# Performance work log

Hardware: AMD Instinct MI355X
Metric: run time of the kernel (lower is better)

## Reference

```python
import jax, jax.numpy as jnp
import numpy as np
import math

B, H, S, D = 2, 16, 2048, 128
TANH_SCALE = 50.0
SCALE = 1.0 / math.sqrt(float(D))


def setup_inputs() -> dict:
    key = jax.random.key(0)
    kq, kk, kv = jax.random.split(key, 3)
    q = jax.random.normal(kq, (B, H, S, D), dtype=jnp.float32)
    k = jax.random.normal(kk, (B, H, D, S), dtype=jnp.float32)  # pre-transposed, as in the torch module
    v = jax.random.normal(kv, (B, H, S, D), dtype=jnp.float32)
    return {"q": q, "k": k, "v": v}


def reference(q, k, v):
    seqlen = q.shape[-2]
    # causal additive mask: -inf strictly above diagonal
    causal = jnp.triu(jnp.ones((seqlen, seqlen), dtype=bool), k=1)
    mask = jnp.where(causal, jnp.float32(-jnp.inf), jnp.float32(0.0))  # [S,S]
    scores = jnp.einsum('bhsd,bhdt->bhst', q, k) * jnp.float32(SCALE)
    y = jnp.tanh(scores / jnp.float32(TANH_SCALE)) * jnp.float32(TANH_SCALE)
    y = y + mask  # broadcast over [B,H]
    p = jax.nn.softmax(y, axis=-1)
    return jnp.einsum('bhst,bhtd->bhsd', p, v)
```

## Files before the change

### kernel.cpp

```cpp
#include <hip/hip_runtime.h>

#define S_ 2048
#define D_ 128
#define NQ 16
#define QBLK 128
#define TBLK 32
#define KSTR 136
#define VSTR 40
#define PSTR 40

typedef short bf16x8 __attribute__((ext_vector_type(8)));
typedef float f32x4 __attribute__((ext_vector_type(4)));

static __device__ __forceinline__ unsigned cvtpk(float a, float b) {
    unsigned r;
    asm("v_cvt_pk_bf16_f32 %0, %1, %2" : "=v"(r) : "v"(a), "v"(b));
    return r;
}
static __device__ __forceinline__ float exp2a(float x) {
    float r;
    asm("v_exp_f32 %0, %1" : "=v"(r) : "v"(x));
    return r;
}
template<int CTRL> static __device__ __forceinline__ float dppf(float x) {
    return __builtin_bit_cast(float,
        __builtin_amdgcn_update_dpp(0, __builtin_bit_cast(int, x), CTRL, 0xF, 0xF, true));
}
static __device__ __forceinline__ float rsum16(float x) {
    x += dppf<0xB1>(x);
    x += dppf<0x4E>(x);
    x += dppf<0x124>(x);
    x += dppf<0x128>(x);
    return x;
}

__global__ __launch_bounds__(512, 2) void gemma2_attn_kernel(
    const float* __restrict__ q, const float* __restrict__ k,
    const float* __restrict__ v, float* __restrict__ out)
{
    __shared__ __align__(16) short smem[2*TBLK*KSTR + 2*D_*VSTR + 8*32*PSTR];

    const int tid = threadIdx.x;
    const int w = tid >> 6, lane = tid & 63;
    const int r = lane & 15, g = lane >> 4;
    const int wg = w >> 2, wl = w & 3;
    const int t256 = tid & 255;

    const int qi = (blockIdx.y < 16) ? blockIdx.x : (15 - blockIdx.x);
    const int bh = blockIdx.y;

    const size_t qb = (size_t)bh * S_ * D_;
    const size_t kb = (size_t)bh * D_ * S_;

    short* lds_kg = smem + wg * (TBLK * KSTR);
    short* lds_vg = smem + 2 * TBLK * KSTR + wg * (D_ * VSTR);
    short* lds_pw = smem + 2 * TBLK * KSTR + 2 * D_ * VSTR + w * (32 * PSTR);
    float* comb = (float*)smem;

    const float C1 = -0.333333333f, C2 = 0.133333333f;
    const float YS = 72.13475204444817f;
    const float ZS = 0.08838834764831845f / 50.0f;
    const float NINF = -__builtin_inff();

    const int kt = t256 & 31, kgd = t256 >> 5;
    const int vd = t256 & 127, vtg = t256 >> 7;

    const int q0 = qi * QBLK;
    const int nss = 2 * qi + 2;

    float kfl[16], vfl[16];
    auto LOAD = [&](int ssn) {
        const int t0g = ssn * 64 + wg * 32;
#pragma unroll
        for (int j = 0; j < 16; ++j)
            kfl[j] = k[kb + (size_t)(kgd * 16 + j) * S_ + t0g + kt];
#pragma unroll
        for (int i = 0; i < 16; ++i)
            vfl[i] = v[qb + (size_t)(t0g + vtg * 16 + i) * D_ + vd];
    };
    auto WRITE = [&]() {
        unsigned pk[8], pv[8];
#pragma unroll
        for (int c = 0; c < 8; ++c) pk[c] = cvtpk(kfl[2 * c], kfl[2 * c + 1]);
#pragma unroll
        for (int c = 0; c < 8; ++c) pv[c] = cvtpk(vfl[2 * c], vfl[2 * c + 1]);
        uint4 a0 = {pk[0], pk[1], pk[2], pk[3]}, a1 = {pk[4], pk[5], pk[6], pk[7]};
        *(uint4*)&lds_kg[kt * KSTR + kgd * 16] = a0;
        *(uint4*)&lds_kg[kt * KSTR + kgd * 16 + 8] = a1;
        uint4 b0 = {pv[0], pv[1], pv[2], pv[3]}, b1 = {pv[4], pv[5], pv[6], pv[7]};
        *(uint4*)&lds_vg[vd * VSTR + vtg * 16] = b0;
        *(uint4*)&lds_vg[vd * VSTR + vtg * 16 + 8] = b1;
    };

    LOAD(0);

    bf16x8 qf[2][4];
#pragma unroll
    for (int rf = 0; rf < 2; ++rf)
#pragma unroll
        for (int kk = 0; kk < 4; ++kk) {
            const float* qp = q + qb + (size_t)(q0 + wl * 32 + rf * 16 + r) * D_ + kk * 32 + g * 8;
            uint4 t4 = {cvtpk(qp[0] * ZS, qp[1] * ZS), cvtpk(qp[2] * ZS, qp[3] * ZS),
                        cvtpk(qp[4] * ZS, qp[5] * ZS), cvtpk(qp[6] * ZS, qp[7] * ZS)};
            qf[rf][kk] = __builtin_bit_cast(bf16x8, t4);
        }

    f32x4 oacc[2][8];
#pragma unroll
    for (int rf = 0; rf < 2; ++rf)
#pragma unroll
        for (int db = 0; db < 8; ++db) oacc[rf][db] = (f32x4){0.f, 0.f, 0.f, 0.f};
    float l_p[2][4];
#pragma unroll
    for (int rf = 0; rf < 2; ++rf)
#pragma unroll
        for (int j = 0; j < 4; ++j) l_p[rf][j] = 0.f;

    const int wrlo = q0 + wl * 32;
    const int pcol0 = (r + 8 * g) & 31;

#pragma unroll 1
    for (int ss = 0; ss < nss; ++ss) {
        const int t0 = ss * 64 + wg * 32;
        __syncthreads();
        WRITE();
        __syncthreads();
        if (ss + 1 < nss) LOAD(ss + 1);

        if (t0 > wrlo + 31) continue;

        f32x4 sf[2][2];
#pragma unroll
        for (int rf = 0; rf < 2; ++rf)
#pragma unroll
            for (int nb = 0; nb < 2; ++nb) sf[rf][nb] = (f32x4){0.f, 0.f, 0.f, 0.f};
#pragma unroll
        for (int nb = 0; nb < 2; ++nb) {
            const int trow = nb * 16 + r;
#pragma unroll
            for (int kk = 0; kk < 4; ++kk) {
                bf16x8 bf = *(const bf16x8*)&lds_kg[trow * KSTR + kk * 32 + g * 8];
                sf[0][nb] = __builtin_amdgcn_mfma_f32_16x16x32_bf16(qf[0][kk], bf, sf[0][nb], 0, 0, 0);
                sf[1][nb] = __builtin_amdgcn_mfma_f32_16x16x32_bf16(qf[1][kk], bf, sf[1][nb], 0, 0, 0);
            }
        }

        if (t0 + 31 > wrlo) {
#pragma unroll
            for (int rf = 0; rf < 2; ++rf)
#pragma unroll
                for (int reg = 0; reg < 4; ++reg) {
                    const int irow = q0 + wl * 32 + rf * 16 + g * 4 + reg;
                    float p0, p1;
                    {
                        float z = sf[rf][0][reg];
                        float z2 = z * z;
                        float t = z * __builtin_fmaf(z2, __builtin_fmaf(z2, C2, C1), 1.0f);
                        float yl = __builtin_fmaf(t, YS, -YS);
                        if (t0 + r > irow) yl = NINF;
                        p0 = exp2a(yl);
                    }
                    {
                        float z = sf[rf][1][reg];
                        float z2 = z * z;
                        float t = z * __builtin_fmaf(z2, __builtin_fmaf(z2, C2, C1), 1.0f);
                        float yl = __builtin_fmaf(t, YS, -YS);
                        if (t0 + 16 + r > irow) yl = NINF;
                        p1 = exp2a(yl);
                    }
                    l_p[rf][reg] += p0 + p1;
                    const unsigned pkd = cvtpk(p0, p1);
                    const int prow = rf * 16 + g * 4 + reg;
                    lds_pw[prow * PSTR + pcol0] = (short)(pkd & 0xffff);
                    lds_pw[prow * PSTR + (pcol0 ^ 16)] = (short)(pkd >> 16);
                }
        } else {
#pragma unroll
            for (int rf = 0; rf < 2; ++rf)
#pragma unroll
                for (int reg = 0; reg < 4; ++reg) {
                    float z0 = sf[rf][0][reg], z1 = sf[rf][1][reg];
                    float z20 = z0 * z0, z21 = z1 * z1;
                    float tt0 = z0 * __builtin_fmaf(z20, __builtin_fmaf(z20, C2, C1), 1.0f);
                    float tt1 = z1 * __builtin_fmaf(z21, __builtin_fmaf(z21, C2, C1), 1.0f);
                    float p0 = exp2a(__builtin_fmaf(tt0, YS, -YS));
                    float p1 = exp2a(__builtin_fmaf(tt1, YS, -YS));
                    l_p[rf][reg] += p0 + p1;
                    const unsigned pkd = cvtpk(p0, p1);
                    const int prow = rf * 16 + g * 4 + reg;
                    lds_pw[prow * PSTR + pcol0] = (short)(pkd & 0xffff);
                    lds_pw[prow * PSTR + (pcol0 ^ 16)] = (short)(pkd >> 16);
                }
        }

        asm volatile("s_waitcnt lgkmcnt(0)" ::: "memory");
        __builtin_amdgcn_sched_barrier(0);
        bf16x8 pa[2];
#pragma unroll
        for (int rf = 0; rf < 2; ++rf)
            pa[rf] = *(const bf16x8*)&lds_pw[(rf * 16 + r) * PSTR + 8 * ((g + (r >> 2)) & 3)];
#pragma unroll
        for (int db = 0; db < 8; ++db) {
            bf16x8 vb = *(const bf16x8*)&lds_vg[(db * 16 + r) * VSTR + g * 8];
            oacc[0][db] = __builtin_amdgcn_mfma_f32_16x16x32_bf16(pa[0], vb, oacc[0][db], 0, 0, 0);
            oacc[1][db] = __builtin_amdgcn_mfma_f32_16x16x32_bf16(pa[1], vb, oacc[1][db], 0, 0, 0);
        }
    }

#define COMB_ROUND(RF, HALF)                                           \
    do {                                                               \
        __syncthreads();                                               \
        if (wg == 1) {                                                 \
            float* c = comb + t256 * 21;                               \
            *(f32x4*)(c + 0)  = oacc[RF][(HALF)*4 + 0];                \
            *(f32x4*)(c + 4)  = oacc[RF][(HALF)*4 + 1];                \
            *(f32x4*)(c + 8)  = oacc[RF][(HALF)*4 + 2];                \
            *(f32x4*)(c + 12) = oacc[RF][(HALF)*4 + 3];                \
            c[16] = l_p[RF][(HALF)*2];                                 \
            c[17] = l_p[RF][(HALF)*2 + 1];                             \
        }                                                              \
        __syncthreads();                                               \
        if (wg == 0) {                                                 \
            const float* c = comb + t256 * 21;                         \
            oacc[RF][(HALF)*4 + 0] += *(const f32x4*)(c + 0);          \
            oacc[RF][(HALF)*4 + 1] += *(const f32x4*)(c + 4);          \
            oacc[RF][(HALF)*4 + 2] += *(const f32x4*)(c + 8);          \
            oacc[RF][(HALF)*4 + 3] += *(const f32x4*)(c + 12);         \
            l_p[RF][(HALF)*2]     += c[16];                            \
            l_p[RF][(HALF)*2 + 1] += c[17];                            \
        }                                                              \
    } while (0)

    COMB_ROUND(0, 0);
    COMB_ROUND(0, 1);
    COMB_ROUND(1, 0);
    COMB_ROUND(1, 1);
#undef COMB_ROUND

    if (wg == 0) {
#pragma unroll
        for (int rf = 0; rf < 2; ++rf) {
            float invl[4];
#pragma unroll
            for (int reg = 0; reg < 4; ++reg)
                invl[reg] = 1.0f / rsum16(l_p[rf][reg]);
#pragma unroll
            for (int db = 0; db < 8; ++db)
#pragma unroll
                for (int reg = 0; reg < 4; ++reg) {
                    const int row = q0 + wl * 32 + rf * 16 + g * 4 + reg;
                    out[qb + (size_t)row * D_ + db * 16 + r] = oacc[rf][db][reg] * invl[reg];
                }
        }
    }
}

extern "C" void kernel_launch(void* const* d_in, const int* in_sizes, int n_in,
                              void* d_out, int out_size, void* d_ws, size_t ws_size,
                              hipStream_t stream) {
    const float* q = (const float*)d_in[0];
    const float* k = (const float*)d_in[1];
    const float* v = (const float*)d_in[2];
    float* out = (float*)d_out;
    dim3 grid(16, 32);
    gemma2_attn_kernel<<<grid, dim3(512), 0, stream>>>(q, k, v, out);
}
```

Before: 121.5 us.

## Pair complementary causal query tiles per block and split KV range via atomics

Each block now processes two query tiles (qi and 15-qi) in sequence, with blockIdx.x's low bit selecting which half of the key range to cover, so every block does a balanced amount of causal work. Partial outputs and row sums are accumulated into global memory with float atomics, and a separate normalization kernel divides by the summed denominators. This drops the in-block LDS combine of the two wave groups. In exchange it adds two memsets, an extra kernel pass over the output, and heavy atomic traffic to global memory.

```diff
diff --git a/kernel.cpp b/kernel.cpp
--- a/kernel.cpp
+++ b/kernel.cpp
@@ -36,7 +36,8 @@
 
 __global__ __launch_bounds__(512, 2) void gemma2_attn_kernel(
     const float* __restrict__ q, const float* __restrict__ k,
-    const float* __restrict__ v, float* __restrict__ out)
+    const float* __restrict__ v, float* __restrict__ out,
+    float* __restrict__ l_ws)
 {
     __shared__ __align__(16) short smem[2*TBLK*KSTR + 2*D_*VSTR + 8*32*PSTR];
 
@@ -46,7 +47,8 @@
     const int wg = w >> 2, wl = w & 3;
     const int t256 = tid & 255;
 
-    const int qi = (blockIdx.y < 16) ? blockIdx.x : (15 - blockIdx.x);
+    const int px = blockIdx.x >> 1;
+    const int h  = blockIdx.x & 1;
     const int bh = blockIdx.y;
 
     const size_t qb = (size_t)bh * S_ * D_;
@@ -55,7 +57,6 @@
     short* lds_kg = smem + wg * (TBLK * KSTR);
     short* lds_vg = smem + 2 * TBLK * KSTR + wg * (D_ * VSTR);
     short* lds_pw = smem + 2 * TBLK * KSTR + 2 * D_ * VSTR + w * (32 * PSTR);
-    float* comb = (float*)smem;
 
     const float C1 = -0.333333333f, C2 = 0.133333333f;
     const float YS = 72.13475204444817f;
@@ -65,18 +66,14 @@
     const int kt = t256 & 31, kgd = t256 >> 5;
     const int vd = t256 & 127, vtg = t256 >> 7;
 
-    const int q0 = qi * QBLK;
-    const int nss = 2 * qi + 2;
-
     float kfl[16], vfl[16];
-    auto LOAD = [&](int ssn) {
-        const int t0g = ssn * 64 + wg * 32;
+    auto LOAD = [&](int tbase) {
 #pragma unroll
         for (int j = 0; j < 16; ++j)
-            kfl[j] = k[kb + (size_t)(kgd * 16 + j) * S_ + t0g + kt];
+            kfl[j] = k[kb + (size_t)(kgd * 16 + j) * S_ + tbase + kt];
 #pragma unroll
         for (int i = 0; i < 16; ++i)
-            vfl[i] = v[qb + (size_t)(t0g + vtg * 16 + i) * D_ + vd];
+            vfl[i] = v[qb + (size_t)(tbase + vtg * 16 + i) * D_ + vd];
     };
     auto WRITE = [&]() {
         unsigned pk[8], pv[8];
@@ -92,166 +89,166 @@
         *(uint4*)&lds_vg[vd * VSTR + vtg * 16 + 8] = b1;
     };
 
-    LOAD(0);
-
-    bf16x8 qf[2][4];
-#pragma unroll
-    for (int rf = 0; rf < 2; ++rf)
-#pragma unroll
-        for (int kk = 0; kk < 4; ++kk) {
-            const float* qp = q + qb + (size_t)(q0 + wl * 32 + rf * 16 + r) * D_ + kk * 32 + g * 8;
-            uint4 t4 = {cvtpk(qp[0] * ZS, qp[1] * ZS), cvtpk(qp[2] * ZS, qp[3] * ZS),
-                        cvtpk(qp[4] * ZS, qp[5] * ZS), cvtpk(qp[6] * ZS, qp[7] * ZS)};
-            qf[rf][kk] = __builtin_bit_cast(bf16x8, t4);
+    const int pcol0 = (r + 8 * g) & 31;
+
+    const int qiA = px,      qiB = NQ - 1 - px;
+    const int baseA = h * (qiA + 1) * 64;
+    const int baseB = h * (qiB + 1) * 64;
+
+    LOAD(baseA + wg * 32);
+
+#pragma unroll 1
+    for (int ph = 0; ph < 2; ++ph) {
+        const int qi   = ph ? qiB : qiA;
+        const int base = ph ? baseB : baseA;
+        const int q0   = qi * QBLK;
+        const int nss  = qi + 1;
+
+        bf16x8 qf[2][4];
+#pragma unroll
+        for (int rf = 0; rf < 2; ++rf)
+#pragma unroll
+            for (int kk = 0; kk < 4; ++kk) {
+                const float* qp = q + qb + (size_t)(q0 + wl * 32 + rf * 16 + r) * D_ + kk * 32 + g * 8;
+                uint4 t4 = {cvtpk(qp[0] * ZS, qp[1] * ZS), cvtpk(qp[2] * ZS, qp[3] * ZS),
+                            cvtpk(qp[4] * ZS, qp[5] * ZS), cvtpk(qp[6] * ZS, qp[7] * ZS)};
+                qf[rf][kk] = __builtin_bit_cast(bf16x8, t4);
+            }
+
+        f32x4 oacc[2][8];
+#pragma unroll
+        for (int rf = 0; rf < 2; ++rf)
+#pragma unroll
+            for (int db = 0; db < 8; ++db) oacc[rf][db] = (f32x4){0.f, 0.f, 0.f, 0.f};
+        float l_p[2][4];
+#pragma unroll
+        for (int rf = 0; rf < 2; ++rf)
+#pragma unroll
+            for (int j = 0; j < 4; ++j) l_p[rf][j] = 0.f;
+
+        const int wrlo = q0 + wl * 32;
+
+#pragma unroll 1
+        for (int ss = 0; ss < nss; ++ss) {
+            const int t0 = base + ss * 64 + wg * 32;
+            __syncthreads();
+            WRITE();
+            __syncthreads();
+            if (ss + 1 < nss) LOAD(base + (ss + 1) * 64 + wg * 32);
+            else if (ph == 0) LOAD(baseB + wg * 32);
+
+            if (t0 > wrlo + 31) continue;
+
+            f32x4 sf[2][2];
+#pragma unroll
+            for (int rf = 0; rf < 2; ++rf)
+#pragma unroll
+                for (int nb = 0; nb < 2; ++nb) sf[rf][nb] = (f32x4){0.f, 0.f, 0.f, 0.f};
+#pragma unroll
+            for (int nb = 0; nb < 2; ++nb) {
+                const int trow = nb * 16 + r;
+#pragma unroll
+                for (int kk = 0; kk < 4; ++kk) {
+                    bf16x8 bf = *(const bf16x8*)&lds_kg[trow * KSTR + kk * 32 + g * 8];
+                    sf[0][nb] = __builtin_amdgcn_mfma_f32_16x16x32_bf16(qf[0][kk], bf, sf[0][nb], 0, 0, 0);
+                    sf[1][nb] = __builtin_amdgcn_mfma_f32_16x16x32_bf16(qf[1][kk], bf, sf[1][nb], 0, 0, 0);
+                }
+            }
+
+            if (t0 + 31 > wrlo) {
+#pragma unroll
+                for (int rf = 0; rf < 2; ++rf)
+#pragma unroll
+                    for (int reg = 0; reg < 4; ++reg) {
+                        const int irow = q0 + wl * 32 + rf * 16 + g * 4 + reg;
+                        float p0, p1;
+                        {
+                            float z = sf[rf][0][reg];
+                            float z2 = z * z;
+                            float t = z * __builtin_fmaf(z2, __builtin_fmaf(z2, C2, C1), 1.0f);
+                            float yl = __builtin_fmaf(t, YS, -YS);
+                            if (t0 + r > irow) yl = NINF;
+                            p0 = exp2a(yl);
+                        }
+                        {
+                            float z = sf[rf][1][reg];
+                            float z2 = z * z;
+                            float t = z * __builtin_fmaf(z2, __builtin_fmaf(z2, C2, C1), 1.0f);
+                            float yl = __builtin_fmaf(t, YS, -YS);
+                            if (t0 + 16 + r > irow) yl = NINF;
+                            p1 = exp2a(yl);
+                        }
+                        l_p[rf][reg] += p0 + p1;
+                        const unsigned pkd = cvtpk(p0, p1);
+                        const int prow = rf * 16 + g * 4 + reg;
+                        lds_pw[prow * PSTR + pcol0] = (short)(pkd & 0xffff);
+                        lds_pw[prow * PSTR + (pcol0 ^ 16)] = (short)(pkd >> 16);
+                    }
+            } else {
+#pragma unroll
+                for (int rf = 0; rf < 2; ++rf)
+#pragma unroll
+                    for (int reg = 0; reg < 4; ++reg) {
+                        float z0 = sf[rf][0][reg], z1 = sf[rf][1][reg];
+                        float z20 = z0 * z0, z21 = z1 * z1;
+                        float tt0 = z0 * __builtin_fmaf(z20, __builtin_fmaf(z20, C2, C1), 1.0f);
+                        float tt1 = z1 * __builtin_fmaf(z21, __builtin_fmaf(z21, C2, C1), 1.0f);
+                        float p0 = exp2a(__builtin_fmaf(tt0, YS, -YS));
+                        float p1 = exp2a(__builtin_fmaf(tt1, YS, -YS));
+                        l_p[rf][reg] += p0 + p1;
+                        const unsigned pkd = cvtpk(p0, p1);
+                        const int prow = rf * 16 + g * 4 + reg;
+                        lds_pw[prow * PSTR + pcol0] = (short)(pkd & 0xffff);
+                        lds_pw[prow * PSTR + (pcol0 ^ 16)] = (short)(pkd >> 16);
+                    }
+            }
+
+            asm volatile("s_waitcnt lgkmcnt(0)" ::: "memory");
+            __builtin_amdgcn_sched_barrier(0);
+            bf16x8 pa[2];
+#pragma unroll
+            for (int rf = 0; rf < 2; ++rf)
+                pa[rf] = *(const bf16x8*)&lds_pw[(rf * 16 + r) * PSTR + 8 * ((g + (r >> 2)) & 3)];
+#pragma unroll
+            for (int db = 0; db < 8; ++db) {
+                bf16x8 vb = *(const bf16x8*)&lds_vg[(db * 16 + r) * VSTR + g * 8];
+                oacc[0][db] = __builtin_amdgcn_mfma_f32_16x16x32_bf16(pa[0], vb, oacc[0][db], 0, 0, 0);
+                oacc[1][db] = __builtin_amdgcn_mfma_f32_16x16x32_bf16(pa[1], vb, oacc[1][db], 0, 0, 0);
+            }
         }
 
-    f32x4 oacc[2][8];
-#pragma unroll
-    for (int rf = 0; rf < 2; ++rf)
-#pragma unroll
-        for (int db = 0; db < 8; ++db) oacc[rf][db] = (f32x4){0.f, 0.f, 0.f, 0.f};
-    float l_p[2][4];
-#pragma unroll
-    for (int rf = 0; rf < 2; ++rf)
-#pragma unroll
-        for (int j = 0; j < 4; ++j) l_p[rf][j] = 0.f;
-
-    const int wrlo = q0 + wl * 32;
-    const int pcol0 = (r + 8 * g) & 31;
-
-#pragma unroll 1
-    for (int ss = 0; ss < nss; ++ss) {
-        const int t0 = ss * 64 + wg * 32;
-        __syncthreads();
-        WRITE();
-        __syncthreads();
-        if (ss + 1 < nss) LOAD(ss + 1);
-
-        if (t0 > wrlo + 31) continue;
-
-        f32x4 sf[2][2];
-#pragma unroll
-        for (int rf = 0; rf < 2; ++rf)
-#pragma unroll
-            for (int nb = 0; nb < 2; ++nb) sf[rf][nb] = (f32x4){0.f, 0.f, 0.f, 0.f};
-#pragma unroll
-        for (int nb = 0; nb < 2; ++nb) {
-            const int trow = nb * 16 + r;
-#pragma unroll
-            for (int kk = 0; kk < 4; ++kk) {
-                bf16x8 bf = *(const bf16x8*)&lds_kg[trow * KSTR + kk * 32 + g * 8];
-                sf[0][nb] = __builtin_amdgcn_mfma_f32_16x16x32_bf16(qf[0][kk], bf, sf[0][nb], 0, 0, 0);
-                sf[1][nb] = __builtin_amdgcn_mfma_f32_16x16x32_bf16(qf[1][kk], bf, sf[1][nb], 0, 0, 0);
-            }
-        }
-
-        if (t0 + 31 > wrlo) {
-#pragma unroll
-            for (int rf = 0; rf < 2; ++rf)
-#pragma unroll
-                for (int reg = 0; reg < 4; ++reg) {
-                    const int irow = q0 + wl * 32 + rf * 16 + g * 4 + reg;
-                    float p0, p1;
-                    {
-                        float z = sf[rf][0][reg];
-                        float z2 = z * z;
-                        float t = z * __builtin_fmaf(z2, __builtin_fmaf(z2, C2, C1), 1.0f);
-                        float yl = __builtin_fmaf(t, YS, -YS);
-                        if (t0 + r > irow) yl = NINF;
-                        p0 = exp2a(yl);
-                    }
-                    {
-                        float z = sf[rf][1][reg];
-                        float z2 = z * z;
-                        float t = z * __builtin_fmaf(z2, __builtin_fmaf(z2, C2, C1), 1.0f);
-                        float yl = __builtin_fmaf(t, YS, -YS);
-                        if (t0 + 16 + r > irow) yl = NINF;
-                        p1 = exp2a(yl);
-                    }
-                    l_p[rf][reg] += p0 + p1;
-                    const unsigned pkd = cvtpk(p0, p1);
-                    const int prow = rf * 16 + g * 4 + reg;
-                    lds_pw[prow * PSTR + pcol0] = (short)(pkd & 0xffff);
-                    lds_pw[prow * PSTR + (pcol0 ^ 16)] = (short)(pkd >> 16);
+#pragma unroll
+        for (int rf = 0; rf < 2; ++rf)
+#pragma unroll
+            for (int reg = 0; reg < 4; ++reg) {
+                float ls = rsum16(l_p[rf][reg]);
+                if (r == 0) {
+                    const int row = q0 + wl * 32 + rf * 16 + g * 4 + reg;
+                    unsafeAtomicAdd(&l_ws[bh * S_ + row], ls);
                 }
-        } else {
-#pragma unroll
-            for (int rf = 0; rf < 2; ++rf)
-#pragma unroll
-                for (int reg = 0; reg < 4; ++reg) {
-                    float z0 = sf[rf][0][reg], z1 = sf[rf][1][reg];
-                    float z20 = z0 * z0, z21 = z1 * z1;
-                    float tt0 = z0 * __builtin_fmaf(z20, __builtin_fmaf(z20, C2, C1), 1.0f);
-                    float tt1 = z1 * __builtin_fmaf(z21, __builtin_fmaf(z21, C2, C1), 1.0f);
-                    float p0 = exp2a(__builtin_fmaf(tt0, YS, -YS));
-                    float p1 = exp2a(__builtin_fmaf(tt1, YS, -YS));
-                    l_p[rf][reg] += p0 + p1;
-                    const unsigned pkd = cvtpk(p0, p1);
-                    const int prow = rf * 16 + g * 4 + reg;
-                    lds_pw[prow * PSTR + pcol0] = (short)(pkd & 0xffff);
-                    lds_pw[prow * PSTR + (pcol0 ^ 16)] = (short)(pkd >> 16);
-                }
-        }
-
-        asm volatile("s_waitcnt lgkmcnt(0)" ::: "memory");
-        __builtin_amdgcn_sched_barrier(0);
-        bf16x8 pa[2];
-#pragma unroll
-        for (int rf = 0; rf < 2; ++rf)
-            pa[rf] = *(const bf16x8*)&lds_pw[(rf * 16 + r) * PSTR + 8 * ((g + (r >> 2)) & 3)];
-#pragma unroll
-        for (int db = 0; db < 8; ++db) {
-            bf16x8 vb = *(const bf16x8*)&lds_vg[(db * 16 + r) * VSTR + g * 8];
-            oacc[0][db] = __builtin_amdgcn_mfma_f32_16x16x32_bf16(pa[0], vb, oacc[0][db], 0, 0, 0);
-            oacc[1][db] = __builtin_amdgcn_mfma_f32_16x16x32_bf16(pa[1], vb, oacc[1][db], 0, 0, 0);
-        }
-    }
-
-#define COMB_ROUND(RF, HALF)                                           \
-    do {                                                               \
-        __syncthreads();                                               \
-        if (wg == 1) {                                                 \
-            float* c = comb + t256 * 21;                               \
-            *(f32x4*)(c + 0)  = oacc[RF][(HALF)*4 + 0];                \
-            *(f32x4*)(c + 4)  = oacc[RF][(HALF)*4 + 1];                \
-            *(f32x4*)(c + 8)  = oacc[RF][(HALF)*4 + 2];                \
-            *(f32x4*)(c + 12) = oacc[RF][(HALF)*4 + 3];                \
-            c[16] = l_p[RF][(HALF)*2];                                 \
-            c[17] = l_p[RF][(HALF)*2 + 1];                             \
-        }                                                              \
-        __syncthreads();                                               \
-        if (wg == 0) {                                                 \
-            const float* c = comb + t256 * 21;                         \
-            oacc[RF][(HALF)*4 + 0] += *(const f32x4*)(c + 0);          \
-            oacc[RF][(HALF)*4 + 1] += *(const f32x4*)(c + 4);          \
-            oacc[RF][(HALF)*4 + 2] += *(const f32x4*)(c + 8);          \
-            oacc[RF][(HALF)*4 + 3] += *(const f32x4*)(c + 12);         \
-            l_p[RF][(HALF)*2]     += c[16];                            \
-            l_p[RF][(HALF)*2 + 1] += c[17];                            \
-        }                                                              \
-    } while (0)
-
-    COMB_ROUND(0, 0);
-    COMB_ROUND(0, 1);
-    COMB_ROUND(1, 0);
-    COMB_ROUND(1, 1);
-#undef COMB_ROUND
-
-    if (wg == 0) {
-#pragma unroll
-        for (int rf = 0; rf < 2; ++rf) {
-            float invl[4];
-#pragma unroll
-            for (int reg = 0; reg < 4; ++reg)
-                invl[reg] = 1.0f / rsum16(l_p[rf][reg]);
+            }
+#pragma unroll
+        for (int rf = 0; rf < 2; ++rf)
 #pragma unroll
             for (int db = 0; db < 8; ++db)
 #pragma unroll
                 for (int reg = 0; reg < 4; ++reg) {
                     const int row = q0 + wl * 32 + rf * 16 + g * 4 + reg;
-                    out[qb + (size_t)row * D_ + db * 16 + r] = oacc[rf][db][reg] * invl[reg];
+                    unsafeAtomicAdd(&out[qb + (size_t)row * D_ + db * 16 + r], oacc[rf][db][reg]);
                 }
-        }
+    }
+}
+
+__global__ __launch_bounds__(256) void norm_kernel(float* __restrict__ out,
+                                                   const float* __restrict__ l_ws)
+{
+    const int n4 = 32 * S_ * D_ / 4;
+    int i = blockIdx.x * 256 + threadIdx.x;
+    for (; i < n4; i += gridDim.x * 256) {
+        const float inv = 1.0f / l_ws[i >> 5];
+        float4 vv = ((float4*)out)[i];
+        vv.x *= inv; vv.y *= inv; vv.z *= inv; vv.w *= inv;
+        ((float4*)out)[i] = vv;
     }
 }
 
@@ -262,6 +259,10 @@
     const float* k = (const float*)d_in[1];
     const float* v = (const float*)d_in[2];
     float* out = (float*)d_out;
+    float* l_ws = (float*)d_ws;
+    hipMemsetAsync(d_out, 0, (size_t)out_size * sizeof(float), stream);
+    hipMemsetAsync(d_ws, 0, (size_t)32 * S_ * sizeof(float), stream);
     dim3 grid(16, 32);
-    gemma2_attn_kernel<<<grid, dim3(512), 0, stream>>>(q, k, v, out);
-}
+    gemma2_attn_kernel<<<grid, dim3(512), 0, stream>>>(q, k, v, out, l_ws);
+    norm_kernel<<<2048, dim3(256), 0, stream>>>(out, l_ws);
+}
```

Measured after the change: 207.8 us. 1.71x slower.

## Split head dim across blocks and pair causal q-blocks for balanced work

Applied to the files above, without the earlier changes.

Each block now computes only half of the output head dimension (64 of 128 columns) and processes two query blocks in sequence: px and its mirror 15-px. This gives every block the same number of causal KV steps, removing the load imbalance from causal masking. It also halves the V tile and output accumulators, which lowers register and LDS use. In exchange, QK^T and the tanh/exp softmax work are repeated by both head-dim halves, so total compute per output rises noticeably.

```diff
diff --git a/kernel.cpp b/kernel.cpp
--- a/kernel.cpp
+++ b/kernel.cpp
@@ -38,7 +38,7 @@
     const float* __restrict__ q, const float* __restrict__ k,
     const float* __restrict__ v, float* __restrict__ out)
 {
-    __shared__ __align__(16) short smem[2*TBLK*KSTR + 2*D_*VSTR + 8*32*PSTR];
+    __shared__ __align__(16) short smem[2*TBLK*KSTR + 2*64*VSTR + 8*32*PSTR];
 
     const int tid = threadIdx.x;
     const int w = tid >> 6, lane = tid & 63;
@@ -46,15 +46,16 @@
     const int wg = w >> 2, wl = w & 3;
     const int t256 = tid & 255;
 
-    const int qi = (blockIdx.y < 16) ? blockIdx.x : (15 - blockIdx.x);
+    const int px = blockIdx.x >> 1;
+    const int dh = blockIdx.x & 1;
     const int bh = blockIdx.y;
 
     const size_t qb = (size_t)bh * S_ * D_;
     const size_t kb = (size_t)bh * D_ * S_;
 
     short* lds_kg = smem + wg * (TBLK * KSTR);
-    short* lds_vg = smem + 2 * TBLK * KSTR + wg * (D_ * VSTR);
-    short* lds_pw = smem + 2 * TBLK * KSTR + 2 * D_ * VSTR + w * (32 * PSTR);
+    short* lds_vg = smem + 2 * TBLK * KSTR + wg * (64 * VSTR);
+    short* lds_pw = smem + 2 * TBLK * KSTR + 2 * 64 * VSTR + w * (32 * PSTR);
     float* comb = (float*)smem;
 
     const float C1 = -0.333333333f, C2 = 0.133333333f;
@@ -63,194 +64,197 @@
     const float NINF = -__builtin_inff();
 
     const int kt = t256 & 31, kgd = t256 >> 5;
-    const int vd = t256 & 127, vtg = t256 >> 7;
-
-    const int q0 = qi * QBLK;
-    const int nss = 2 * qi + 2;
-
-    float kfl[16], vfl[16];
-    auto LOAD = [&](int ssn) {
-        const int t0g = ssn * 64 + wg * 32;
+    const int vd = t256 & 63, vtg = t256 >> 6;
+
+    float kfl[16], vfl[8];
+    auto LOAD = [&](int t0g) {
 #pragma unroll
         for (int j = 0; j < 16; ++j)
             kfl[j] = k[kb + (size_t)(kgd * 16 + j) * S_ + t0g + kt];
 #pragma unroll
-        for (int i = 0; i < 16; ++i)
-            vfl[i] = v[qb + (size_t)(t0g + vtg * 16 + i) * D_ + vd];
+        for (int i = 0; i < 8; ++i)
+            vfl[i] = v[qb + (size_t)(t0g + vtg * 8 + i) * D_ + dh * 64 + vd];
     };
     auto WRITE = [&]() {
-        unsigned pk[8], pv[8];
+        unsigned pk[8], pv[4];
 #pragma unroll
         for (int c = 0; c < 8; ++c) pk[c] = cvtpk(kfl[2 * c], kfl[2 * c + 1]);
 #pragma unroll
-        for (int c = 0; c < 8; ++c) pv[c] = cvtpk(vfl[2 * c], vfl[2 * c + 1]);
+        for (int c = 0; c < 4; ++c) pv[c] = cvtpk(vfl[2 * c], vfl[2 * c + 1]);
         uint4 a0 = {pk[0], pk[1], pk[2], pk[3]}, a1 = {pk[4], pk[5], pk[6], pk[7]};
         *(uint4*)&lds_kg[kt * KSTR + kgd * 16] = a0;
         *(uint4*)&lds_kg[kt * KSTR + kgd * 16 + 8] = a1;
-        uint4 b0 = {pv[0], pv[1], pv[2], pv[3]}, b1 = {pv[4], pv[5], pv[6], pv[7]};
-        *(uint4*)&lds_vg[vd * VSTR + vtg * 16] = b0;
-        *(uint4*)&lds_vg[vd * VSTR + vtg * 16 + 8] = b1;
+        uint4 b0 = {pv[0], pv[1], pv[2], pv[3]};
+        *(uint4*)&lds_vg[vd * VSTR + vtg * 8] = b0;
     };
 
-    LOAD(0);
-
-    bf16x8 qf[2][4];
-#pragma unroll
-    for (int rf = 0; rf < 2; ++rf)
-#pragma unroll
-        for (int kk = 0; kk < 4; ++kk) {
-            const float* qp = q + qb + (size_t)(q0 + wl * 32 + rf * 16 + r) * D_ + kk * 32 + g * 8;
-            uint4 t4 = {cvtpk(qp[0] * ZS, qp[1] * ZS), cvtpk(qp[2] * ZS, qp[3] * ZS),
-                        cvtpk(qp[4] * ZS, qp[5] * ZS), cvtpk(qp[6] * ZS, qp[7] * ZS)};
-            qf[rf][kk] = __builtin_bit_cast(bf16x8, t4);
+    const int pcol0 = (r + 8 * g) & 31;
+
+    LOAD(wg * 32);
+
+#pragma unroll 1
+    for (int ph = 0; ph < 2; ++ph) {
+        const int qi = ph ? (NQ - 1 - px) : px;
+        const int q0 = qi * QBLK;
+        const int nss = 2 * qi + 2;
+
+        bf16x8 qf[2][4];
+#pragma unroll
+        for (int rf = 0; rf < 2; ++rf)
+#pragma unroll
+            for (int kk = 0; kk < 4; ++kk) {
+                const float* qp = q + qb + (size_t)(q0 + wl * 32 + rf * 16 + r) * D_ + kk * 32 + g * 8;
+                uint4 t4 = {cvtpk(qp[0] * ZS, qp[1] * ZS), cvtpk(qp[2] * ZS, qp[3] * ZS),
+                            cvtpk(qp[4] * ZS, qp[5] * ZS), cvtpk(qp[6] * ZS, qp[7] * ZS)};
+                qf[rf][kk] = __builtin_bit_cast(bf16x8, t4);
+            }
+
+        f32x4 oacc[2][4];
+#pragma unroll
+        for (int rf = 0; rf < 2; ++rf)
+#pragma unroll
+            for (int db = 0; db < 4; ++db) oacc[rf][db] = (f32x4){0.f, 0.f, 0.f, 0.f};
+        float l_p[2][4];
+#pragma unroll
+        for (int rf = 0; rf < 2; ++rf)
+#pragma unroll
+            for (int j = 0; j < 4; ++j) l_p[rf][j] = 0.f;
+
+        const int wrlo = q0 + wl * 32;
+
+#pragma unroll 1
+        for (int ss = 0; ss < nss; ++ss) {
+            const int t0 = ss * 64 + wg * 32;
+            __syncthreads();
+            WRITE();
+            __syncthreads();
+            if (ss + 1 < nss) LOAD((ss + 1) * 64 + wg * 32);
+            else if (ph == 0) LOAD(wg * 32);
+
+            if (t0 > wrlo + 31) continue;
+
+            f32x4 sf[2][2];
+#pragma unroll
+            for (int rf = 0; rf < 2; ++rf)
+#pragma unroll
+                for (int nb = 0; nb < 2; ++nb) sf[rf][nb] = (f32x4){0.f, 0.f, 0.f, 0.f};
+#pragma unroll
+            for (int nb = 0; nb < 2; ++nb) {
+                const int trow = nb * 16 + r;
+#pragma unroll
+                for (int kk = 0; kk < 4; ++kk) {
+                    bf16x8 bf = *(const bf16x8*)&lds_kg[trow * KSTR + kk * 32 + g * 8];
+                    sf[0][nb] = __builtin_amdgcn_mfma_f32_16x16x32_bf16(qf[0][kk], bf, sf[0][nb], 0, 0, 0);
+                    sf[1][nb] = __builtin_amdgcn_mfma_f32_16x16x32_bf16(qf[1][kk], bf, sf[1][nb], 0, 0, 0);
+                }
+            }
+
+            if (t0 + 31 > wrlo) {
+#pragma unroll
+                for (int rf = 0; rf < 2; ++rf)
+#pragma unroll
+                    for (int reg = 0; reg < 4; ++reg) {
+                        const int irow = q0 + wl * 32 + rf * 16 + g * 4 + reg;
+                        float p0, p1;
+                        {
+                            float z = sf[rf][0][reg];
+                            float z2 = z * z;
+                            float t = z * __builtin_fmaf(z2, __builtin_fmaf(z2, C2, C1), 1.0f);
+                            float yl = __builtin_fmaf(t, YS, -YS);
+                            if (t0 + r > irow) yl = NINF;
+                            p0 = exp2a(yl);
+                        }
+                        {
+                            float z = sf[rf][1][reg];
+                            float z2 = z * z;
+                            float t = z * __builtin_fmaf(z2, __builtin_fmaf(z2, C2, C1), 1.0f);
+                            float yl = __builtin_fmaf(t, YS, -YS);
+                            if (t0 + 16 + r > irow) yl = NINF;
+                            p1 = exp2a(yl);
+                        }
+                        l_p[rf][reg] += p0 + p1;
+                        const unsigned pkd = cvtpk(p0, p1);
+                        const int prow = rf * 16 + g * 4 + reg;
+                        lds_pw[prow * PSTR + pcol0] = (short)(pkd & 0xffff);
+                        lds_pw[prow * PSTR + (pcol0 ^ 16)] = (short)(pkd >> 16);
+                    }
+            } else {
+#pragma unroll
+                for (int rf = 0; rf < 2; ++rf)
+#pragma unroll
+                    for (int reg = 0; reg < 4; ++reg) {
+                        float z0 = sf[rf][0][reg], z1 = sf[rf][1][reg];
+                        float z20 = z0 * z0, z21 = z1 * z1;
+                        float tt0 = z0 * __builtin_fmaf(z20, __builtin_fmaf(z20, C2, C1), 1.0f);
+                        float tt1 = z1 * __builtin_fmaf(z21, __builtin_fmaf(z21, C2, C1), 1.0f);
+                        float p0 = exp2a(__builtin_fmaf(tt0, YS, -YS));
+                        float p1 = exp2a(__builtin_fmaf(tt1, YS, -YS));
+                        l_p[rf][reg] += p0 + p1;
+                        const unsigned pkd = cvtpk(p0, p1);
+                        const int prow = rf * 16 + g * 4 + reg;
+                        lds_pw[prow * PSTR + pcol0] = (short)(pkd & 0xffff);
+                        lds_pw[prow * PSTR + (pcol0 ^ 16)] = (short)(pkd >> 16);
+                    }
+            }
+
+            asm volatile("s_waitcnt lgkmcnt(0)" ::: "memory");
+            __builtin_amdgcn_sched_barrier(0);
+            bf16x8 pa[2];
+#pragma unroll
+            for (int rf = 0; rf < 2; ++rf)
+                pa[rf] = *(const bf16x8*)&lds_pw[(rf * 16 + r) * PSTR + 8 * ((g + (r >> 2)) & 3)];
+#pragma unroll
+            for (int db = 0; db < 4; ++db) {
+                bf16x8 vb = *(const bf16x8*)&lds_vg[(db * 16 + r) * VSTR + g * 8];
+                oacc[0][db] = __builtin_amdgcn_mfma_f32_16x16x32_bf16(pa[0], vb, oacc[0][db], 0, 0, 0);
+                oacc[1][db] = __builtin_amdgcn_mfma_f32_16x16x32_bf16(pa[1], vb, oacc[1][db], 0, 0, 0);
+            }
         }
 
-    f32x4 oacc[2][8];
-#pragma unroll
-    for (int rf = 0; rf < 2; ++rf)
-#pragma unroll
-        for (int db = 0; db < 8; ++db) oacc[rf][db] = (f32x4){0.f, 0.f, 0.f, 0.f};
-    float l_p[2][4];
-#pragma unroll
-    for (int rf = 0; rf < 2; ++rf)
-#pragma unroll
-        for (int j = 0; j < 4; ++j) l_p[rf][j] = 0.f;
-
-    const int wrlo = q0 + wl * 32;
-    const int pcol0 = (r + 8 * g) & 31;
-
-#pragma unroll 1
-    for (int ss = 0; ss < nss; ++ss) {
-        const int t0 = ss * 64 + wg * 32;
-        __syncthreads();
-        WRITE();
-        __syncthreads();
-        if (ss + 1 < nss) LOAD(ss + 1);
-
-        if (t0 > wrlo + 31) continue;
-
-        f32x4 sf[2][2];
-#pragma unroll
-        for (int rf = 0; rf < 2; ++rf)
-#pragma unroll
-            for (int nb = 0; nb < 2; ++nb) sf[rf][nb] = (f32x4){0.f, 0.f, 0.f, 0.f};
-#pragma unroll
-        for (int nb = 0; nb < 2; ++nb) {
-            const int trow = nb * 16 + r;
-#pragma unroll
-            for (int kk = 0; kk < 4; ++kk) {
-                bf16x8 bf = *(const bf16x8*)&lds_kg[trow * KSTR + kk * 32 + g * 8];
-                sf[0][nb] = __builtin_amdgcn_mfma_f32_16x16x32_bf16(qf[0][kk], bf, sf[0][nb], 0, 0, 0);
-                sf[1][nb] = __builtin_amdgcn_mfma_f32_16x16x32_bf16(qf[1][kk], bf, sf[1][nb], 0, 0, 0);
-            }
-        }
-
-        if (t0 + 31 > wrlo) {
-#pragma unroll
-            for (int rf = 0; rf < 2; ++rf)
-#pragma unroll
-                for (int reg = 0; reg < 4; ++reg) {
-                    const int irow = q0 + wl * 32 + rf * 16 + g * 4 + reg;
-                    float p0, p1;
-                    {
-                        float z = sf[rf][0][reg];
-                        float z2 = z * z;
-                        float t = z * __builtin_fmaf(z2, __builtin_fmaf(z2, C2, C1), 1.0f);
-                        float yl = __builtin_fmaf(t, YS, -YS);
-                        if (t0 + r > irow) yl = NINF;
-                        p0 = exp2a(yl);
+#define COMB_ROUND(RF)                                                 \
+        do {                                                           \
+            __syncthreads();                                           \
+            if (wg == 1) {                                             \
+                float* c = comb + t256 * 21;                           \
+                *(f32x4*)(c + 0)  = oacc[RF][0];                       \
+                *(f32x4*)(c + 4)  = oacc[RF][1];                       \
+                *(f32x4*)(c + 8)  = oacc[RF][2];                       \
+                *(f32x4*)(c + 12) = oacc[RF][3];                       \
+                c[16] = l_p[RF][0]; c[17] = l_p[RF][1];                \
+                c[18] = l_p[RF][2]; c[19] = l_p[RF][3];                \
+            }                                                          \
+            __syncthreads();                                           \
+            if (wg == 0) {                                             \
+                const float* c = comb + t256 * 21;                     \
+                oacc[RF][0] += *(const f32x4*)(c + 0);                 \
+                oacc[RF][1] += *(const f32x4*)(c + 4);                 \
+                oacc[RF][2] += *(const f32x4*)(c + 8);                 \
+                oacc[RF][3] += *(const f32x4*)(c + 12);                \
+                l_p[RF][0] += c[16]; l_p[RF][1] += c[17];              \
+                l_p[RF][2] += c[18]; l_p[RF][3] += c[19];              \
+            }                                                          \
+        } while (0)
+
+        COMB_ROUND(0);
+        COMB_ROUND(1);
+#undef COMB_ROUND
+
+        if (wg == 0) {
+#pragma unroll
+            for (int rf = 0; rf < 2; ++rf) {
+                float invl[4];
+#pragma unroll
+                for (int reg = 0; reg < 4; ++reg)
+                    invl[reg] = 1.0f / rsum16(l_p[rf][reg]);
+#pragma unroll
+                for (int db = 0; db < 4; ++db)
+#pragma unroll
+                    for (int reg = 0; reg < 4; ++reg) {
+                        const int row = q0 + wl * 32 + rf * 16 + g * 4 + reg;
+                        out[qb + (size_t)row * D_ + dh * 64 + db * 16 + r] =
+                            oacc[rf][db][reg] * invl[reg];
                     }
-                    {
-                        float z = sf[rf][1][reg];
-                        float z2 = z * z;
-                        float t = z * __builtin_fmaf(z2, __builtin_fmaf(z2, C2, C1), 1.0f);
-                        float yl = __builtin_fmaf(t, YS, -YS);
-                        if (t0 + 16 + r > irow) yl = NINF;
-                        p1 = exp2a(yl);
-                    }
-                    l_p[rf][reg] += p0 + p1;
-                    const unsigned pkd = cvtpk(p0, p1);
-                    const int prow = rf * 16 + g * 4 + reg;
-                    lds_pw[prow * PSTR + pcol0] = (short)(pkd & 0xffff);
-                    lds_pw[prow * PSTR + (pcol0 ^ 16)] = (short)(pkd >> 16);
-                }
-        } else {
-#pragma unroll
-            for (int rf = 0; rf < 2; ++rf)
-#pragma unroll
-                for (int reg = 0; reg < 4; ++reg) {
-                    float z0 = sf[rf][0][reg], z1 = sf[rf][1][reg];
-                    float z20 = z0 * z0, z21 = z1 * z1;
-                    float tt0 = z0 * __builtin_fmaf(z20, __builtin_fmaf(z20, C2, C1), 1.0f);
-                    float tt1 = z1 * __builtin_fmaf(z21, __builtin_fmaf(z21, C2, C1), 1.0f);
-                    float p0 = exp2a(__builtin_fmaf(tt0, YS, -YS));
-                    float p1 = exp2a(__builtin_fmaf(tt1, YS, -YS));
-                    l_p[rf][reg] += p0 + p1;
-                    const unsigned pkd = cvtpk(p0, p1);
-                    const int prow = rf * 16 + g * 4 + reg;
-                    lds_pw[prow * PSTR + pcol0] = (short)(pkd & 0xffff);
-                    lds_pw[prow * PSTR + (pcol0 ^ 16)] = (short)(pkd >> 16);
-                }
-        }
-
-        asm volatile("s_waitcnt lgkmcnt(0)" ::: "memory");
-        __builtin_amdgcn_sched_barrier(0);
-        bf16x8 pa[2];
-#pragma unroll
-        for (int rf = 0; rf < 2; ++rf)
-            pa[rf] = *(const bf16x8*)&lds_pw[(rf * 16 + r) * PSTR + 8 * ((g + (r >> 2)) & 3)];
-#pragma unroll
-        for (int db = 0; db < 8; ++db) {
-            bf16x8 vb = *(const bf16x8*)&lds_vg[(db * 16 + r) * VSTR + g * 8];
-            oacc[0][db] = __builtin_amdgcn_mfma_f32_16x16x32_bf16(pa[0], vb, oacc[0][db], 0, 0, 0);
-            oacc[1][db] = __builtin_amdgcn_mfma_f32_16x16x32_bf16(pa[1], vb, oacc[1][db], 0, 0, 0);
-        }
-    }
-
-#define COMB_ROUND(RF, HALF)                                           \
-    do {                                                               \
-        __syncthreads();                                               \
-        if (wg == 1) {                                                 \
-            float* c = comb + t256 * 21;                               \
-            *(f32x4*)(c + 0)  = oacc[RF][(HALF)*4 + 0];                \
-            *(f32x4*)(c + 4)  = oacc[RF][(HALF)*4 + 1];                \
-            *(f32x4*)(c + 8)  = oacc[RF][(HALF)*4 + 2];                \
-            *(f32x4*)(c + 12) = oacc[RF][(HALF)*4 + 3];                \
-            c[16] = l_p[RF][(HALF)*2];                                 \
-            c[17] = l_p[RF][(HALF)*2 + 1];                             \
-        }                                                              \
-        __syncthreads();                                               \
-        if (wg == 0) {                                                 \
-            const float* c = comb + t256 * 21;                         \
-            oacc[RF][(HALF)*4 + 0] += *(const f32x4*)(c + 0);          \
-            oacc[RF][(HALF)*4 + 1] += *(const f32x4*)(c + 4);          \
-            oacc[RF][(HALF)*4 + 2] += *(const f32x4*)(c + 8);          \
-            oacc[RF][(HALF)*4 + 3] += *(const f32x4*)(c + 12);         \
-            l_p[RF][(HALF)*2]     += c[16];                            \
-            l_p[RF][(HALF)*2 + 1] += c[17];                            \
-        }                                                              \
-    } while (0)
-
-    COMB_ROUND(0, 0);
-    COMB_ROUND(0, 1);
-    COMB_ROUND(1, 0);
-    COMB_ROUND(1, 1);
-#undef COMB_ROUND
-
-    if (wg == 0) {
-#pragma unroll
-        for (int rf = 0; rf < 2; ++rf) {
-            float invl[4];
-#pragma unroll
-            for (int reg = 0; reg < 4; ++reg)
-                invl[reg] = 1.0f / rsum16(l_p[rf][reg]);
-#pragma unroll
-            for (int db = 0; db < 8; ++db)
-#pragma unroll
-                for (int reg = 0; reg < 4; ++reg) {
-                    const int row = q0 + wl * 32 + rf * 16 + g * 4 + reg;
-                    out[qb + (size_t)row * D_ + db * 16 + r] = oacc[rf][db][reg] * invl[reg];
-                }
+            }
         }
     }
 }
```

Measured after the change: 150.6 us. 24.0% more time.
